# Kernel optimization log

Hardware: AMD Instinct MI355X
Metric: run time of the kernel (lower is better)

Reference implementation:

```python
import jax, jax.numpy as jnp
import numpy as np

N_NODES = 100000
N_EDGES = 3200000
K_STEPS = 10
ALPHA = 0.1


def setup_inputs() -> dict:
    key = jax.random.key(0)
    k1, k2, k3, k4 = jax.random.split(key, 4)
    x = jax.random.normal(k1, (N_NODES, 512), dtype=jnp.float32)
    edge_index = jax.random.randint(k2, (2, N_EDGES), 0, N_NODES, dtype=jnp.int32)
    # Glorot-ish scaled params for lin1/lin2
    W1 = jax.random.normal(k3, (512, 256), dtype=jnp.float32) * (1.0 / np.sqrt(512))
    b1 = jnp.zeros((256,), dtype=jnp.float32)
    W2 = jax.random.normal(k4, (256, 64), dtype=jnp.float32) * (1.0 / np.sqrt(256))
    b2 = jnp.zeros((64,), dtype=jnp.float32)
    return {"x": x, "edge_index": edge_index, "W1": W1, "b1": b1, "W2": W2, "b2": b2}


def _gcn_norm(edge_index, num_nodes):
    # Add self-loops, compute symmetric normalization coefficients (PyG gcn_norm).
    loop = jnp.arange(num_nodes, dtype=edge_index.dtype)
    row = jnp.concatenate([edge_index[0], loop])
    col = jnp.concatenate([edge_index[1], loop])
    deg = jax.ops.segment_sum(jnp.ones_like(col, dtype=jnp.float32), col,
                              num_segments=num_nodes)
    dinv = jnp.where(deg > 0, jax.lax.rsqrt(deg), 0.0)
    norm = dinv[row] * dinv[col]  # [E + N]
    return row, col, norm


def reference(x, edge_index, W1, b1, W2, b2):
    # Inference mode: dropout is identity (training=False).
    h = jax.nn.relu(x @ W1 + b1) @ W2 + b2  # [N, out]
    num_nodes = x.shape[0]
    row, col, norm = _gcn_norm(edge_index, num_nodes)

    def step(z, _):
        msg = norm[:, None] * z[row]  # gather + scale, [E+N, out]
        agg = jax.ops.segment_sum(msg, col, num_segments=num_nodes)
        return (1.0 - ALPHA) * agg + ALPHA * h, None

    z, _ = jax.lax.scan(step, h, None, length=K_STEPS)
    return jax.nn.log_softmax(z, axis=1)
```

## Files before the change

### kernel.cpp

```cpp
#include <hip/hip_runtime.h>
#include <hip/hip_bf16.h>

typedef __attribute__((ext_vector_type(8))) short   short8;
typedef __attribute__((ext_vector_type(4))) short   shortx4;
typedef __attribute__((ext_vector_type(8))) __bf16  bf16x8;
typedef __attribute__((ext_vector_type(4))) float   floatx4;

__device__ inline float bf2f(short u) {
    return __builtin_bit_cast(float, (unsigned)((unsigned short)u) << 16);
}
__device__ inline short f2bf(float f) {
    return __builtin_bit_cast(short, __float2bfloat16(f));
}

__device__ inline void gll16(const void* g, void* l) {
    __builtin_amdgcn_global_load_lds(
        (const __attribute__((address_space(1))) unsigned int*)g,
        (__attribute__((address_space(3))) unsigned int*)l, 16, 0, 0);
}


__global__ void count_kernel(const int* __restrict__ col, int* __restrict__ icnt, int E) {
    int e = blockIdx.x * 256 + threadIdx.x;
    if (e < E) atomicAdd(&icnt[col[e]], 1);
}

__global__ void dinv_cursor_kernel(const int* __restrict__ icnt, float* __restrict__ dinv,
                                   int* __restrict__ cursor, int N) {
    int i = blockIdx.x * 256 + threadIdx.x;
    if (i < N) { dinv[i] = rsqrtf((float)(icnt[i] + 1)); cursor[i] = 0; }
}

__global__ __launch_bounds__(1024) void scan_kernel(const int* __restrict__ icnt,
                                                    int* __restrict__ offs, int N) {
    __shared__ int part[1024];
    int t = threadIdx.x;
    int CH = (N + 1023) >> 10;
    int base = t * CH;
    int s = 0;
    for (int i = 0; i < CH; i++) { int idx = base + i; if (idx < N) s += icnt[idx]; }
    part[t] = s;
    __syncthreads();
    for (int o = 1; o < 1024; o <<= 1) {
        int u = (t >= o) ? part[t - o] : 0;
        __syncthreads();
        part[t] += u;
        __syncthreads();
    }
    int off = part[t] - s;
    for (int i = 0; i < CH; i++) {
        int idx = base + i;
        if (idx < N) { offs[idx] = off; off += icnt[idx]; }
    }
    if (t == 1023) offs[N] = part[1023];
}

__global__ void scatter_kernel(const int* __restrict__ row, const int* __restrict__ col,
                               const int* __restrict__ offs, int* __restrict__ cursor,
                               int* __restrict__ csr, int E) {
    int e = blockIdx.x * 256 + threadIdx.x;
    if (e < E) {
        int c = col[e];
        int p = offs[c] + atomicAdd(&cursor[c], 1);
        csr[p] = row[e];
    }
}


__global__ void w1_tile_kernel(const float* __restrict__ src,
                               __hip_bfloat16* __restrict__ dst) {
    int t = blockIdx.x * 256 + threadIdx.x;
    if (t < 512 * 256) {
        int k = t >> 8, n = t & 255;
        int kc = k >> 5, kl = k & 31;
        int slot = kl >> 3, pos = kl & 7;
        int sl = slot ^ ((n >> 1) & 3);
        dst[kc * 8192 + n * 32 + sl * 8 + pos] = __float2bfloat16(src[t]);
    }
}

__global__ void transpose_cvt_kernel(const float* __restrict__ src,
                                     __hip_bfloat16* __restrict__ dst, int K, int N) {
    int t = blockIdx.x * 256 + threadIdx.x;
    if (t < K * N) { int k = t / N, n = t % N; dst[n * K + k] = __float2bfloat16(src[t]); }
}


__global__ __launch_bounds__(256) void mlp_kernel(
    const float* __restrict__ x, const __hip_bfloat16* __restrict__ W1Tt,
    const float* __restrict__ b1, const __hip_bfloat16* __restrict__ W2T,
    const float* __restrict__ b2, __hip_bfloat16* __restrict__ h, int M)
{
    __shared__ __align__(16) short lds[16384];
    short* Ts = lds;

    const int t = threadIdx.x;
    const int lane = t & 63, wave = t >> 6;
    const int lm = lane & 15, quad = lane >> 4;
    const int block_m = blockIdx.x * 64;
    const short* w2s = (const short*)W2T;
    const char*  w1b = (const char*)W1Tt;

    const int grow = block_m + wave * 16 + lm;
    const bool rok = grow < M;
    const float* xrow = x + (size_t)grow * 512 + quad * 8;
    const floatx4 z4 = (floatx4){0.f, 0.f, 0.f, 0.f};

    const int chunk_base = wave * 4;
    const int gl_off = lane * 16;

    auto stageB = [&](int kc, int buf) {
#pragma unroll
        for (int it = 0; it < 4; it++) {
            int chunk = chunk_base + it;
            gll16(w1b + (size_t)kc * 16384 + chunk * 1024 + gl_off,
                  &lds[buf * 8192 + chunk * 512]);
        }
    };

    floatx4 accA[16];
#pragma unroll
    for (int i = 0; i < 16; i++) accA[i] = z4;

    stageB(0, 0);
    floatx4 a0  = rok ? *(const floatx4*)xrow       : z4;
    floatx4 a1  = rok ? *(const floatx4*)(xrow + 4) : z4;
    floatx4 na0 = z4, na1 = z4;

    const int boff = lm * 32 + ((quad ^ ((lm >> 1) & 3)) << 3);

    __syncthreads();

    for (int kc = 0; kc < 16; kc++) {
        if (kc < 15) {
            stageB(kc + 1, (kc + 1) & 1);
            const float* p = xrow + (kc + 1) * 32;
            na0 = rok ? *(const floatx4*)p       : z4;
            na1 = rok ? *(const floatx4*)(p + 4) : z4;
        }
        short8 afs;
#pragma unroll
        for (int j = 0; j < 4; j++) { afs[j] = f2bf(a0[j]); afs[4 + j] = f2bf(a1[j]); }
        bf16x8 af = __builtin_bit_cast(bf16x8, afs);
        const short* bb = &lds[(kc & 1) * 8192];
#pragma unroll
        for (int nt = 0; nt < 16; nt++) {
            bf16x8 bfr = __builtin_bit_cast(bf16x8, *(const short8*)&bb[nt * 512 + boff]);
            accA[nt] = __builtin_amdgcn_mfma_f32_16x16x32_bf16(af, bfr, accA[nt], 0, 0, 0);
        }
        a0 = na0; a1 = na1;
        __syncthreads();
    }

    floatx4 accB[4];
#pragma unroll
    for (int j = 0; j < 4; j++) accB[j] = z4;

#pragma unroll
    for (int s = 0; s < 4; s++) {
        __syncthreads();
#pragma unroll
        for (int ntl = 0; ntl < 4; ntl++) {
            int nt = s * 4 + ntl;
            float bv = b1[nt * 16 + lm];
#pragma unroll
            for (int r = 0; r < 4; r++) {
                int rowl = wave * 16 + quad * 4 + r;
                Ts[rowl * 72 + ntl * 16 + lm] = f2bf(fmaxf(accA[nt][r] + bv, 0.f));
            }
        }
        __syncthreads();
#pragma unroll
        for (int kk = 0; kk < 2; kk++) {
            bf16x8 af2 = __builtin_bit_cast(bf16x8,
                *(const short8*)&Ts[(wave * 16 + lm) * 72 + kk * 32 + quad * 8]);
#pragma unroll
            for (int nt = 0; nt < 4; nt++) {
                bf16x8 bfr = __builtin_bit_cast(bf16x8,
                    *(const short8*)&w2s[(size_t)(nt * 16 + lm) * 256 + s * 64 + kk * 32 + quad * 8]);
                accB[nt] = __builtin_amdgcn_mfma_f32_16x16x32_bf16(af2, bfr, accB[nt], 0, 0, 0);
            }
        }
    }

#pragma unroll
    for (int nt = 0; nt < 4; nt++) {
        int colg = nt * 16 + lm;
        float bv = b2[colg];
#pragma unroll
        for (int r = 0; r < 4; r++) {
            int rowg = block_m + wave * 16 + quad * 4 + r;
            if (rowg < M)
                h[(size_t)rowg * 64 + colg] = __float2bfloat16(accB[nt][r] + bv);
        }
    }
}


__global__ __launch_bounds__(256) void prop_kernel(
    const __hip_bfloat16* __restrict__ z_in, const __hip_bfloat16* __restrict__ h,
    const float* __restrict__ dinv, const int* __restrict__ offs,
    const int* __restrict__ csr, __hip_bfloat16* __restrict__ z_out,
    float* __restrict__ out, int N, int last)
{
    int node = blockIdx.x * 4 + (threadIdx.x >> 6);
    if (node >= N) return;
    int lane = threadIdx.x & 63;
    int g = lane >> 3, i = lane & 7;
    const short* zs = (const short*)z_in;
    const short* hs = (const short*)h;
    float di = dinv[node];
    int s = offs[node], e = offs[node + 1];
    float acc[8] = {0.f, 0.f, 0.f, 0.f, 0.f, 0.f, 0.f, 0.f};

    for (int j0 = s; j0 < e; j0 += 64) {
        int jj = j0 + lane;
        int nbr = 0; float dn = 0.f;
        if (jj < e) { nbr = csr[jj]; dn = dinv[nbr]; }
        int cnt = min(64, e - j0);
        int tmax = (cnt + 7) >> 3;
        for (int tt = 0; tt < tmax; tt++) {
            int src = tt * 8 + g;
            int nb = __shfl(nbr, src);
            float wv = __shfl(dn, src);
            short8 zv = *(const short8*)&zs[(size_t)nb * 64 + i * 8];
#pragma unroll
            for (int j = 0; j < 8; j++)
                acc[j] = fmaf(wv, bf2f(zv[j]), acc[j]);
        }
    }
#pragma unroll
    for (int j = 0; j < 8; j++) {
        acc[j] += __shfl_xor(acc[j], 8);
        acc[j] += __shfl_xor(acc[j], 16);
        acc[j] += __shfl_xor(acc[j], 32);
    }

    short8 zv = *(const short8*)&zs[(size_t)node * 64 + i * 8];
    short8 hv = *(const short8*)&hs[(size_t)node * 64 + i * 8];
    float v[8];
#pragma unroll
    for (int j = 0; j < 8; j++)
        v[j] = 0.9f * (di * acc[j] + di * di * bf2f(zv[j])) + 0.1f * bf2f(hv[j]);

    if (!last) {
        if (g == 0) {
            short8 o8;
#pragma unroll
            for (int j = 0; j < 8; j++) o8[j] = f2bf(v[j]);
            *(short8*)&((short*)z_out)[(size_t)node * 64 + i * 8] = o8;
        }
    } else {
        float m = v[0];
#pragma unroll
        for (int j = 1; j < 8; j++) m = fmaxf(m, v[j]);
        m = fmaxf(m, __shfl_xor(m, 1));
        m = fmaxf(m, __shfl_xor(m, 2));
        m = fmaxf(m, __shfl_xor(m, 4));
        float ss = 0.f;
#pragma unroll
        for (int j = 0; j < 8; j++) ss += expf(v[j] - m);
        ss += __shfl_xor(ss, 1);
        ss += __shfl_xor(ss, 2);
        ss += __shfl_xor(ss, 4);
        float ls = m + logf(ss);
        if (g == 0) {
            floatx4 o0, o1;
#pragma unroll
            for (int j = 0; j < 4; j++) { o0[j] = v[j] - ls; o1[j] = v[4 + j] - ls; }
            *(floatx4*)&out[(size_t)node * 64 + i * 8]     = o0;
            *(floatx4*)&out[(size_t)node * 64 + i * 8 + 4] = o1;
        }
    }
}


extern "C" void kernel_launch(void* const* d_in, const int* in_sizes, int n_in,
                              void* d_out, int out_size, void* d_ws, size_t ws_size,
                              hipStream_t stream) {
    const float* x  = (const float*)d_in[0];
    const int*   ei = (const int*)d_in[1];
    const float* W1 = (const float*)d_in[2];
    const float* b1 = (const float*)d_in[3];
    const float* W2 = (const float*)d_in[4];
    const float* b2 = (const float*)d_in[5];
    float* out = (float*)d_out;

    const int FIN = 512, FH = 256, FO = 64;
    const int N = in_sizes[0] / FIN;
    const int E = in_sizes[1] / 2;
    const int* erow = ei;
    const int* ecol = ei + E;

    char* w = (char*)d_ws;
    size_t o = 0;
    auto take = [&](size_t bytes) -> void* {
        void* p = w + o;
        o += (bytes + 511) & ~(size_t)511;
        return p;
    };
    int*   icnt   = (int*)  take((size_t)N * 4);
    float* dinv   = (float*)take((size_t)N * 4);
    int*   offs   = (int*)  take((size_t)(N + 1) * 4);
    int*   cursor = (int*)  take((size_t)N * 4);
    int*   csr    = (int*)  take((size_t)E * 4);
    __hip_bfloat16* W1Tt = (__hip_bfloat16*)take((size_t)FIN * FH * 2);
    __hip_bfloat16* W2T  = (__hip_bfloat16*)take((size_t)FH * FO * 2);
    __hip_bfloat16* hbuf = (__hip_bfloat16*)take((size_t)N * FO * 2);
    __hip_bfloat16* zA   = (__hip_bfloat16*)take((size_t)N * FO * 2);
    __hip_bfloat16* zB   = (__hip_bfloat16*)out;

    (void)hipMemsetAsync(icnt, 0, (size_t)N * 4, stream);
    count_kernel<<<(E + 255) / 256, 256, 0, stream>>>(ecol, icnt, E);
    dinv_cursor_kernel<<<(N + 255) / 256, 256, 0, stream>>>(icnt, dinv, cursor, N);
    scan_kernel<<<1, 1024, 0, stream>>>(icnt, offs, N);
    scatter_kernel<<<(E + 255) / 256, 256, 0, stream>>>(erow, ecol, offs, cursor, csr, E);
    w1_tile_kernel<<<(FIN * FH + 255) / 256, 256, 0, stream>>>(W1, W1Tt);
    transpose_cvt_kernel<<<(FH * FO + 255) / 256, 256, 0, stream>>>(W2, W2T, FH, FO);

    mlp_kernel<<<(N + 63) / 64, 256, 0, stream>>>(x, W1Tt, b1, W2T, b2, hbuf, N);

    const __hip_bfloat16* zin = hbuf;
    for (int k = 0; k < 10; k++) {
        int last = (k == 9);
        __hip_bfloat16* zout = (k & 1) ? zB : zA;
        prop_kernel<<<(N + 3) / 4, 256, 0, stream>>>(zin, hbuf, dinv, offs, csr,
                                                     zout, out, N, last);
        zin = zout;
    }
}
```

Baseline: 1.441 ms.

## Replace single-block prefix scan with three-pass multi-block scan

The degree prefix scan used to build the CSR offsets ran in one 1024-thread block, where each thread walked a strided chunk of about 98 entries serially. It is now split into a per-block reduction, a single small block that scans the block sums, and a per-block local scan that writes the offsets. This spreads the work over about 98 blocks with coalesced loads, at the cost of two extra kernel launches. The middle pass assumes at most 128 blocks, which limits N to about 131k nodes.

```diff
diff --git a/kernel.cpp b/kernel.cpp
--- a/kernel.cpp
+++ b/kernel.cpp
@@ -31,28 +31,72 @@
     if (i < N) { dinv[i] = rsqrtf((float)(icnt[i] + 1)); cursor[i] = 0; }
 }
 
-__global__ __launch_bounds__(1024) void scan_kernel(const int* __restrict__ icnt,
-                                                    int* __restrict__ offs, int N) {
-    __shared__ int part[1024];
+
+__global__ __launch_bounds__(256) void blocksum_kernel(const int* __restrict__ icnt,
+                                                       int* __restrict__ bsum, int N) {
+    int b = blockIdx.x, t = threadIdx.x;
+    int base = b * 1024 + t * 4;
+    int s = 0;
+    if (base + 3 < N) {
+        int4 v = *(const int4*)&icnt[base];
+        s = v.x + v.y + v.z + v.w;
+    } else {
+        for (int i = 0; i < 4; i++) if (base + i < N) s += icnt[base + i];
+    }
+    __shared__ int red[256];
+    red[t] = s;
+    __syncthreads();
+    for (int o = 128; o > 0; o >>= 1) {
+        if (t < o) red[t] += red[t + o];
+        __syncthreads();
+    }
+    if (t == 0) bsum[b] = red[0];
+}
+
+__global__ __launch_bounds__(128) void bscan_kernel(int* __restrict__ bsum,
+                                                    int* __restrict__ offs, int NB, int N) {
+    __shared__ int sh[128];
     int t = threadIdx.x;
-    int CH = (N + 1023) >> 10;
-    int base = t * CH;
-    int s = 0;
-    for (int i = 0; i < CH; i++) { int idx = base + i; if (idx < N) s += icnt[idx]; }
-    part[t] = s;
+    int v = (t < NB) ? bsum[t] : 0;
+    sh[t] = v;
     __syncthreads();
-    for (int o = 1; o < 1024; o <<= 1) {
-        int u = (t >= o) ? part[t - o] : 0;
-        __syncthreads();
-        part[t] += u;
-        __syncthreads();
-    }
-    int off = part[t] - s;
-    for (int i = 0; i < CH; i++) {
+    for (int o = 1; o < 128; o <<= 1) {
+        int u = (t >= o) ? sh[t - o] : 0;
+        __syncthreads();
+        sh[t] += u;
+        __syncthreads();
+    }
+    if (t < NB) bsum[t] = sh[t] - v;
+    if (t == 127) offs[N] = sh[127];
+}
+
+__global__ __launch_bounds__(256) void offs_kernel(const int* __restrict__ icnt,
+                                                   const int* __restrict__ bsum,
+                                                   int* __restrict__ offs, int N) {
+    int b = blockIdx.x, t = threadIdx.x;
+    int base = b * 1024 + t * 4;
+    int v[4]; int s = 0;
+#pragma unroll
+    for (int i = 0; i < 4; i++) {
         int idx = base + i;
-        if (idx < N) { offs[idx] = off; off += icnt[idx]; }
-    }
-    if (t == 1023) offs[N] = part[1023];
+        v[i] = (idx < N) ? icnt[idx] : 0;
+        s += v[i];
+    }
+    __shared__ int sh[256];
+    sh[t] = s;
+    __syncthreads();
+    for (int o = 1; o < 256; o <<= 1) {
+        int u = (t >= o) ? sh[t - o] : 0;
+        __syncthreads();
+        sh[t] += u;
+        __syncthreads();
+    }
+    int off = bsum[b] + sh[t] - s;
+#pragma unroll
+    for (int i = 0; i < 4; i++) {
+        int idx = base + i;
+        if (idx < N) { offs[idx] = off; off += v[i]; }
+    }
 }
 
 __global__ void scatter_kernel(const int* __restrict__ row, const int* __restrict__ col,
@@ -304,16 +348,21 @@
     int*   offs   = (int*)  take((size_t)(N + 1) * 4);
     int*   cursor = (int*)  take((size_t)N * 4);
     int*   csr    = (int*)  take((size_t)E * 4);
+    int*   bsum   = (int*)  take((size_t)128 * 4);
     __hip_bfloat16* W1Tt = (__hip_bfloat16*)take((size_t)FIN * FH * 2);
     __hip_bfloat16* W2T  = (__hip_bfloat16*)take((size_t)FH * FO * 2);
     __hip_bfloat16* hbuf = (__hip_bfloat16*)take((size_t)N * FO * 2);
     __hip_bfloat16* zA   = (__hip_bfloat16*)take((size_t)N * FO * 2);
     __hip_bfloat16* zB   = (__hip_bfloat16*)out;
 
+    const int NB = (N + 1023) / 1024;
+
     (void)hipMemsetAsync(icnt, 0, (size_t)N * 4, stream);
     count_kernel<<<(E + 255) / 256, 256, 0, stream>>>(ecol, icnt, E);
     dinv_cursor_kernel<<<(N + 255) / 256, 256, 0, stream>>>(icnt, dinv, cursor, N);
-    scan_kernel<<<1, 1024, 0, stream>>>(icnt, offs, N);
+    blocksum_kernel<<<NB, 256, 0, stream>>>(icnt, bsum, N);
+    bscan_kernel<<<1, 128, 0, stream>>>(bsum, offs, NB, N);
+    offs_kernel<<<NB, 256, 0, stream>>>(icnt, bsum, offs, N);
     scatter_kernel<<<(E + 255) / 256, 256, 0, stream>>>(erow, ecol, offs, cursor, csr, E);
     w1_tile_kernel<<<(FIN * FH + 255) / 256, 256, 0, stream>>>(W1, W1Tt);
     transpose_cvt_kernel<<<(FH * FO + 255) / 256, 256, 0, stream>>>(W2, W2T, FH, FO);
```

Result: faster. 1.265 ms (-12.2%).
